# Kernel tuning notes

Measured on AMD Instinct MI355X. Metric: run time of the kernel, lower is better.

The kernel has to match this reference:

```python
import jax, jax.numpy as jnp
import numpy as np

B, D = 1024, 512


def setup_inputs() -> dict:
    key = jax.random.key(0)
    k_a, k_b, k_w, k_bias = jax.random.split(key, 4)
    a = jax.random.normal(k_a, (B, D), dtype=jnp.float32)
    b = jax.random.normal(k_b, (B, D), dtype=jnp.float32)
    # nn.Linear(input_dim, output_dim): weight [out, in], bias [out]
    bound = 1.0 / np.sqrt(D)
    W = jax.random.uniform(k_w, (D, D), dtype=jnp.float32, minval=-bound, maxval=bound)
    bias = jax.random.uniform(k_bias, (D,), dtype=jnp.float32, minval=-bound, maxval=bound)
    return {"a": a, "b": b, "W": W, "bias": bias}


def reference(a, b, W, bias):
    # attention(): weights[bt,i,j] = b[bt,i] * a[bt,j]  (rank-1 outer product, [B,D,D])
    logits = b[:, :, None] * a[:, None, :]           # [B, D, D]
    sm = jax.nn.softmax(logits, axis=1)              # softmax over dim=1 (the i axis)
    # bmm(a[B,1,D], weights^T) -> out[bt,j] = sum_k a[bt,k] * sm[bt,j,k]
    attn_out = jnp.einsum('bk,bjk->bj', a, sm)       # [B, D]
    # dropout in eval mode == identity; fc + residual
    return a + attn_out @ W.T + bias
```

## Files before the change

### kernel.cpp

```cpp
#include <hip/hip_runtime.h>

#define D 512
#define LOG2E 1.44269504088896340736f

#if defined(__has_builtin)
#if __has_builtin(__builtin_amdgcn_exp2f)
#define EXP2(x) __builtin_amdgcn_exp2f(x)
#else
#define EXP2(x) exp2f(x)
#endif
#else
#define EXP2(x) exp2f(x)
#endif

__global__ __launch_bounds__(256) void attn_kernel(
    const float* __restrict__ a, const float* __restrict__ b,
    float* __restrict__ attn) {
  __shared__ float c_s[D];
  const int bt = blockIdx.x;
  const int tid = threadIdx.x;
  const float* __restrict__ ap = a + (size_t)bt * D;
  const float* __restrict__ bp = b + (size_t)bt * D;

#pragma unroll
  for (int kk = 0; kk < 2; ++kk) {
    const int k = tid + kk * 256;
    const float ak_raw = ap[k];
    const float ak = ak_raw * LOG2E;
    float z0 = 0.f, z1 = 0.f, z2 = 0.f, z3 = 0.f;
#pragma unroll 4
    for (int i = 0; i < D; i += 4) {
      z0 += EXP2(bp[i + 0] * ak);
      z1 += EXP2(bp[i + 1] * ak);
      z2 += EXP2(bp[i + 2] * ak);
      z3 += EXP2(bp[i + 3] * ak);
    }
    c_s[k] = ak_raw / ((z0 + z1) + (z2 + z3));
  }
  __syncthreads();

#pragma unroll
  for (int jj = 0; jj < 2; ++jj) {
    const int j = tid + jj * 256;
    const float bj = bp[j] * LOG2E;
    float s0 = 0.f, s1 = 0.f, s2 = 0.f, s3 = 0.f;
#pragma unroll 4
    for (int k = 0; k < D; k += 4) {
      const float4 c4 = *(const float4*)&c_s[k];
      s0 = fmaf(c4.x, EXP2(ap[k + 0] * bj), s0);
      s1 = fmaf(c4.y, EXP2(ap[k + 1] * bj), s1);
      s2 = fmaf(c4.z, EXP2(ap[k + 2] * bj), s2);
      s3 = fmaf(c4.w, EXP2(ap[k + 3] * bj), s3);
    }
    attn[(size_t)bt * D + j] = (s0 + s1) + (s2 + s3);
  }
}

__global__ __launch_bounds__(256) void out_kernel(
    const float* __restrict__ attn, const float* __restrict__ W,
    const float* __restrict__ a, const float* __restrict__ bias,
    float* __restrict__ out) {
  __shared__ float As[32][68];
  __shared__ float Bs[32][68];
  const int tid = threadIdx.x;
  const int bx = blockIdx.x;
  const int by = blockIdx.y;
  const int tx = tid & 15;
  const int ty = tid >> 4;
  float acc[4][4] = {};

  for (int k0 = 0; k0 < D; k0 += 32) {
#pragma unroll
    for (int xx = 0; xx < 2; ++xx) {
      const int x = tid + xx * 256;
      const int r = x >> 3;
      const int c4 = x & 7;
      const float4 va =
          *(const float4*)(attn + (size_t)(by * 64 + r) * D + k0 + c4 * 4);
      const float4 vw =
          *(const float4*)(W + (size_t)(bx * 64 + r) * D + k0 + c4 * 4);
      As[c4 * 4 + 0][r] = va.x;
      As[c4 * 4 + 1][r] = va.y;
      As[c4 * 4 + 2][r] = va.z;
      As[c4 * 4 + 3][r] = va.w;
      Bs[c4 * 4 + 0][r] = vw.x;
      Bs[c4 * 4 + 1][r] = vw.y;
      Bs[c4 * 4 + 2][r] = vw.z;
      Bs[c4 * 4 + 3][r] = vw.w;
    }
    __syncthreads();
#pragma unroll
    for (int kk = 0; kk < 32; ++kk) {
      const float4 af = *(const float4*)&As[kk][ty * 4];
      const float4 bf = *(const float4*)&Bs[kk][tx * 4];
      const float afv[4] = {af.x, af.y, af.z, af.w};
      const float bfv[4] = {bf.x, bf.y, bf.z, bf.w};
#pragma unroll
      for (int i = 0; i < 4; ++i)
#pragma unroll
        for (int j = 0; j < 4; ++j) acc[i][j] = fmaf(afv[i], bfv[j], acc[i][j]);
    }
    __syncthreads();
  }

  const int n = bx * 64 + tx * 4;
  const float4 bv = *(const float4*)(bias + n);
#pragma unroll
  for (int i = 0; i < 4; ++i) {
    const int m = by * 64 + ty * 4 + i;
    const float4 av = *(const float4*)(a + (size_t)m * D + n);
    float4 o;
    o.x = av.x + acc[i][0] + bv.x;
    o.y = av.y + acc[i][1] + bv.y;
    o.z = av.z + acc[i][2] + bv.z;
    o.w = av.w + acc[i][3] + bv.w;
    *(float4*)(out + (size_t)m * D + n) = o;
  }
}

extern "C" void kernel_launch(void* const* d_in, const int* in_sizes, int n_in,
                              void* d_out, int out_size, void* d_ws,
                              size_t ws_size, hipStream_t stream) {
  const float* a = (const float*)d_in[0];
  const float* b = (const float*)d_in[1];
  const float* W = (const float*)d_in[2];
  const float* bias = (const float*)d_in[3];
  float* out = (float*)d_out;
  float* attn = (float*)d_ws;

  attn_kernel<<<1024, 256, 0, stream>>>(a, b, attn);
  out_kernel<<<dim3(8, 16), 256, 0, stream>>>(attn, W, a, bias, out);
}
```

Before: 150.6 us.

## Compute softmax exponentials once per tile in fp16 LDS; split-K GEMM with atomics

The attention kernel used to evaluate each exponential twice, once for the column sums and once for the weighted output. It now computes each exp once per 64-column tile, shifted by a bound from the max/min of b, and stores the values as half2 in swizzled shared memory. The column sums and the weighted sum then reuse those stored values, which roughly halves the transcendental work. The output GEMM is split along K into 4 slices that accumulate with atomicAdd into an output pre-filled with a+bias by a new init kernel, to raise the block count. The trade-offs are fp16 rounding of the exponentials, nondeterministic float atomics and an extra kernel launch.

```diff
diff --git a/kernel.cpp b/kernel.cpp
--- a/kernel.cpp
+++ b/kernel.cpp
@@ -1,6 +1,9 @@
 #include <hip/hip_runtime.h>
+#include <hip/hip_fp16.h>
 
 #define D 512
+#define KT 64
+#define NT 8
 #define LOG2E 1.44269504088896340736f
 
 #if defined(__has_builtin)
@@ -13,63 +16,168 @@
 #define EXP2(x) exp2f(x)
 #endif
 
-__global__ __launch_bounds__(256) void attn_kernel(
+union H2U { __half2 h; unsigned int u; };
+
+__device__ __forceinline__ unsigned int pkh(float lo, float hi) {
+  H2U p; p.h = __float22half2_rn(make_float2(lo, hi));
+  return p.u;
+}
+__device__ __forceinline__ float2 uph(unsigned int u) {
+  H2U p; p.u = u;
+  return __half22float2(p.h);
+}
+
+__global__ __launch_bounds__(256, 2) void attn_kernel(
     const float* __restrict__ a, const float* __restrict__ b,
     float* __restrict__ attn) {
-  __shared__ float c_s[D];
+  __shared__ unsigned int E[D * KT / 2];
+  __shared__ float a_s[D];
+  __shared__ float zred[32 * 68];
+  __shared__ float c_s[KT];
+  __shared__ float red[8];
+
   const int bt = blockIdx.x;
   const int tid = threadIdx.x;
   const float* __restrict__ ap = a + (size_t)bt * D;
   const float* __restrict__ bp = b + (size_t)bt * D;
 
-#pragma unroll
-  for (int kk = 0; kk < 2; ++kk) {
-    const int k = tid + kk * 256;
-    const float ak_raw = ap[k];
-    const float ak = ak_raw * LOG2E;
+  {
+    float2 va = *(const float2*)(ap + tid * 2);
+    a_s[tid * 2] = va.x;
+    a_s[tid * 2 + 1] = va.y;
+  }
+
+  const int k8 = tid & 7;
+  const int jp = tid >> 3;
+
+  float breg[16];
+#pragma unroll
+  for (int jj = 0; jj < 16; ++jj) breg[jj] = bp[jj * 32 + jp];
+
+  float bmax = breg[0], bmin = breg[0];
+#pragma unroll
+  for (int jj = 1; jj < 16; ++jj) {
+    bmax = fmaxf(bmax, breg[jj]);
+    bmin = fminf(bmin, breg[jj]);
+  }
+#pragma unroll
+  for (int off = 32; off; off >>= 1) {
+    bmax = fmaxf(bmax, __shfl_xor(bmax, off));
+    bmin = fminf(bmin, __shfl_xor(bmin, off));
+  }
+  if ((tid & 63) == 0) {
+    red[tid >> 6] = bmax;
+    red[4 + (tid >> 6)] = bmin;
+  }
+  __syncthreads();
+  bmax = fmaxf(fmaxf(red[0], red[1]), fmaxf(red[2], red[3]));
+  bmin = fminf(fminf(red[4], red[5]), fminf(red[6], red[7]));
+
+  float at0a = 0.f, at0b = 0.f, at1a = 0.f, at1b = 0.f;
+  const int jr0 = tid;
+  const int jr1 = tid + 256;
+  const int sw = jr0 & 7;
+
+  for (int t = 0; t < NT; ++t) {
+    const int k0 = t * KT;
+    float alk[8], m2[8];
+#pragma unroll
+    for (int c = 0; c < 8; ++c) {
+      const float ar = a_s[k0 + k8 * 8 + c];
+      const float al = ar * LOG2E;
+      alk[c] = al;
+      m2[c] = -al * (ar > 0.f ? bmax : bmin);
+    }
     float z0 = 0.f, z1 = 0.f, z2 = 0.f, z3 = 0.f;
-#pragma unroll 4
-    for (int i = 0; i < D; i += 4) {
-      z0 += EXP2(bp[i + 0] * ak);
-      z1 += EXP2(bp[i + 1] * ak);
-      z2 += EXP2(bp[i + 2] * ak);
-      z3 += EXP2(bp[i + 3] * ak);
-    }
-    c_s[k] = ak_raw / ((z0 + z1) + (z2 + z3));
-  }
-  __syncthreads();
-
-#pragma unroll
-  for (int jj = 0; jj < 2; ++jj) {
-    const int j = tid + jj * 256;
-    const float bj = bp[j] * LOG2E;
-    float s0 = 0.f, s1 = 0.f, s2 = 0.f, s3 = 0.f;
-#pragma unroll 4
-    for (int k = 0; k < D; k += 4) {
-      const float4 c4 = *(const float4*)&c_s[k];
-      s0 = fmaf(c4.x, EXP2(ap[k + 0] * bj), s0);
-      s1 = fmaf(c4.y, EXP2(ap[k + 1] * bj), s1);
-      s2 = fmaf(c4.z, EXP2(ap[k + 2] * bj), s2);
-      s3 = fmaf(c4.w, EXP2(ap[k + 3] * bj), s3);
-    }
-    attn[(size_t)bt * D + j] = (s0 + s1) + (s2 + s3);
-  }
-}
-
-__global__ __launch_bounds__(256) void out_kernel(
+    float z4 = 0.f, z5 = 0.f, z6 = 0.f, z7 = 0.f;
+
+#pragma unroll
+    for (int jj = 0; jj < 16; ++jj) {
+      const int j = jj * 32 + jp;
+      const float bj = breg[jj];
+      const float e0 = EXP2(fmaf(alk[0], bj, m2[0]));
+      const float e1 = EXP2(fmaf(alk[1], bj, m2[1]));
+      const float e2 = EXP2(fmaf(alk[2], bj, m2[2]));
+      const float e3 = EXP2(fmaf(alk[3], bj, m2[3]));
+      const float e4 = EXP2(fmaf(alk[4], bj, m2[4]));
+      const float e5 = EXP2(fmaf(alk[5], bj, m2[5]));
+      const float e6 = EXP2(fmaf(alk[6], bj, m2[6]));
+      const float e7 = EXP2(fmaf(alk[7], bj, m2[7]));
+      z0 += e0; z1 += e1; z2 += e2; z3 += e3;
+      z4 += e4; z5 += e5; z6 += e6; z7 += e7;
+      uint4 u;
+      u.x = pkh(e0, e1);
+      u.y = pkh(e2, e3);
+      u.z = pkh(e4, e5);
+      u.w = pkh(e6, e7);
+      *((uint4*)((char*)E + j * 128 + ((k8 ^ (j & 7)) * 16))) = u;
+    }
+    {
+      float* zp = &zred[jp * 68 + k8 * 8];
+      *(float4*)zp = make_float4(z0, z1, z2, z3);
+      *(float4*)(zp + 4) = make_float4(z4, z5, z6, z7);
+    }
+    __syncthreads();
+    if (tid < KT) {
+      float Z = 0.f;
+#pragma unroll
+      for (int p = 0; p < 32; ++p) Z += zred[p * 68 + tid];
+      c_s[tid] = a_s[k0 + tid] / Z;
+    }
+    __syncthreads();
+
+#pragma unroll
+    for (int g = 0; g < 8; ++g) {
+      const float4 c0 = *(const float4*)&c_s[g * 8];
+      const float4 c1 = *(const float4*)&c_s[g * 8 + 4];
+      const int pg = (g ^ sw) * 16;
+      const uint4 u0 = *(const uint4*)((const char*)E + jr0 * 128 + pg);
+      const uint4 u1 = *(const uint4*)((const char*)E + jr1 * 128 + pg);
+      float2 f;
+      f = uph(u0.x); at0a = fmaf(f.x, c0.x, at0a); at0b = fmaf(f.y, c0.y, at0b);
+      f = uph(u0.y); at0a = fmaf(f.x, c0.z, at0a); at0b = fmaf(f.y, c0.w, at0b);
+      f = uph(u0.z); at0a = fmaf(f.x, c1.x, at0a); at0b = fmaf(f.y, c1.y, at0b);
+      f = uph(u0.w); at0a = fmaf(f.x, c1.z, at0a); at0b = fmaf(f.y, c1.w, at0b);
+      f = uph(u1.x); at1a = fmaf(f.x, c0.x, at1a); at1b = fmaf(f.y, c0.y, at1b);
+      f = uph(u1.y); at1a = fmaf(f.x, c0.z, at1a); at1b = fmaf(f.y, c0.w, at1b);
+      f = uph(u1.z); at1a = fmaf(f.x, c1.x, at1a); at1b = fmaf(f.y, c1.y, at1b);
+      f = uph(u1.w); at1a = fmaf(f.x, c1.z, at1a); at1b = fmaf(f.y, c1.w, at1b);
+    }
+    __syncthreads();
+  }
+  attn[(size_t)bt * D + jr0] = at0a + at0b;
+  attn[(size_t)bt * D + jr1] = at1a + at1b;
+}
+
+__global__ __launch_bounds__(256) void init_out(const float* __restrict__ a,
+                                                const float* __restrict__ bias,
+                                                float* __restrict__ out) {
+  const int g = blockIdx.x * 256 + threadIdx.x;
+  const float4 av = ((const float4*)a)[g];
+  const float4 bv = ((const float4*)bias)[g & 127];
+  float4 o;
+  o.x = av.x + bv.x;
+  o.y = av.y + bv.y;
+  o.z = av.z + bv.z;
+  o.w = av.w + bv.w;
+  ((float4*)out)[g] = o;
+}
+
+__global__ __launch_bounds__(256) void gemm_kernel(
     const float* __restrict__ attn, const float* __restrict__ W,
-    const float* __restrict__ a, const float* __restrict__ bias,
     float* __restrict__ out) {
   __shared__ float As[32][68];
   __shared__ float Bs[32][68];
   const int tid = threadIdx.x;
   const int bx = blockIdx.x;
   const int by = blockIdx.y;
+  const int bz = blockIdx.z;
   const int tx = tid & 15;
   const int ty = tid >> 4;
   float acc[4][4] = {};
 
-  for (int k0 = 0; k0 < D; k0 += 32) {
+  const int kbeg = bz * 128;
+  for (int k0 = kbeg; k0 < kbeg + 128; k0 += 32) {
 #pragma unroll
     for (int xx = 0; xx < 2; ++xx) {
       const int x = tid + xx * 256;
@@ -104,17 +212,13 @@
   }
 
   const int n = bx * 64 + tx * 4;
-  const float4 bv = *(const float4*)(bias + n);
 #pragma unroll
   for (int i = 0; i < 4; ++i) {
-    const int m = by * 64 + ty * 4 + i;
-    const float4 av = *(const float4*)(a + (size_t)m * D + n);
-    float4 o;
-    o.x = av.x + acc[i][0] + bv.x;
-    o.y = av.y + acc[i][1] + bv.y;
-    o.z = av.z + acc[i][2] + bv.z;
-    o.w = av.w + acc[i][3] + bv.w;
-    *(float4*)(out + (size_t)m * D + n) = o;
+    float* op = out + (size_t)(by * 64 + ty * 4 + i) * D + n;
+    atomicAdd(op + 0, acc[i][0]);
+    atomicAdd(op + 1, acc[i][1]);
+    atomicAdd(op + 2, acc[i][2]);
+    atomicAdd(op + 3, acc[i][3]);
   }
 }
 
@@ -128,6 +232,7 @@
   float* out = (float*)d_out;
   float* attn = (float*)d_ws;
 
+  init_out<<<512, 256, 0, stream>>>(a, bias, out);
   attn_kernel<<<1024, 256, 0, stream>>>(a, b, attn);
-  out_kernel<<<dim3(8, 16), 256, 0, stream>>>(attn, W, a, bias, out);
-}
+  gemm_kernel<<<dim3(8, 16, 4), 256, 0, stream>>>(attn, W, out);
+}
```

After: 151.0 us. Within noise of the previous version (+0.2%).

## Compute each softmax exponential once and reuse for normaliser and weighted sum

Applied to the files above, without the earlier changes.

Restructures the attention kernel so each thread computes exp2 values for a 64-wide k tile, keeping them in registers. The same values feed both the column normaliser, reduced across threads through shared memory, and the weighted accumulation into output rows. This removes the second full pass of exponentials. The fc GEMM is retiled to 32x32 output tiles with 64-deep k steps, launching more blocks. In exchange there is high register pressure from the cached exponentials and extra barriers per tile.

```diff
diff --git a/kernel.cpp b/kernel.cpp
--- a/kernel.cpp
+++ b/kernel.cpp
@@ -1,6 +1,8 @@
 #include <hip/hip_runtime.h>
 
 #define D 512
+#define KT 64
+#define NT 8
 #define LOG2E 1.44269504088896340736f
 
 #if defined(__has_builtin)
@@ -13,108 +15,153 @@
 #define EXP2(x) exp2f(x)
 #endif
 
-__global__ __launch_bounds__(256) void attn_kernel(
+__global__ __launch_bounds__(256, 2) void attn_kernel(
     const float* __restrict__ a, const float* __restrict__ b,
     float* __restrict__ attn) {
-  __shared__ float c_s[D];
+  __shared__ float a_s[D];
+  __shared__ float zred[32 * 68];
+  __shared__ float c_s[KT];
+  __shared__ float attn_s[D];
+
   const int bt = blockIdx.x;
   const int tid = threadIdx.x;
   const float* __restrict__ ap = a + (size_t)bt * D;
   const float* __restrict__ bp = b + (size_t)bt * D;
 
+  {
+    float2 va = *(const float2*)(ap + tid * 2);
+    a_s[tid * 2] = va.x;
+    a_s[tid * 2 + 1] = va.y;
+  }
+
+  const int k8 = tid & 7;
+  const int jp = tid >> 3;
+
+  float breg[16];
 #pragma unroll
-  for (int kk = 0; kk < 2; ++kk) {
-    const int k = tid + kk * 256;
-    const float ak_raw = ap[k];
-    const float ak = ak_raw * LOG2E;
-    float z0 = 0.f, z1 = 0.f, z2 = 0.f, z3 = 0.f;
-#pragma unroll 4
-    for (int i = 0; i < D; i += 4) {
-      z0 += EXP2(bp[i + 0] * ak);
-      z1 += EXP2(bp[i + 1] * ak);
-      z2 += EXP2(bp[i + 2] * ak);
-      z3 += EXP2(bp[i + 3] * ak);
+  for (int jj = 0; jj < 16; ++jj) breg[jj] = bp[jj * 32 + jp];
+
+  float part[16];
+#pragma unroll
+  for (int jj = 0; jj < 16; ++jj) part[jj] = 0.f;
+
+  __syncthreads();
+
+  for (int t = 0; t < NT; ++t) {
+    const int k0 = t * KT;
+    float alk[8];
+#pragma unroll
+    for (int c = 0; c < 8; ++c) alk[c] = a_s[k0 + k8 * 8 + c] * LOG2E;
+
+    float e[16][8];
+    float z[8];
+#pragma unroll
+    for (int c = 0; c < 8; ++c) z[c] = 0.f;
+
+#pragma unroll
+    for (int jj = 0; jj < 16; ++jj) {
+      const float bj = breg[jj];
+#pragma unroll
+      for (int c = 0; c < 8; ++c) {
+        const float ev = EXP2(alk[c] * bj);
+        e[jj][c] = ev;
+        z[c] += ev;
+      }
     }
-    c_s[k] = ak_raw / ((z0 + z1) + (z2 + z3));
+    {
+      float* zp = &zred[jp * 68 + k8 * 8];
+      *(float4*)zp = make_float4(z[0], z[1], z[2], z[3]);
+      *(float4*)(zp + 4) = make_float4(z[4], z[5], z[6], z[7]);
+    }
+    __syncthreads();
+    if (tid < KT) {
+      float Z = 0.f;
+#pragma unroll
+      for (int p = 0; p < 32; ++p) Z += zred[p * 68 + tid];
+      c_s[tid] = a_s[k0 + tid] / Z;
+    }
+    __syncthreads();
+
+    float cs[8];
+    *(float4*)&cs[0] = *(const float4*)&c_s[k8 * 8];
+    *(float4*)&cs[4] = *(const float4*)&c_s[k8 * 8 + 4];
+#pragma unroll
+    for (int jj = 0; jj < 16; ++jj) {
+#pragma unroll
+      for (int c = 0; c < 8; ++c) part[jj] = fmaf(cs[c], e[jj][c], part[jj]);
+    }
+  }
+
+#pragma unroll
+  for (int jj = 0; jj < 16; ++jj) {
+    float v = part[jj];
+    v += __shfl_xor(v, 1);
+    v += __shfl_xor(v, 2);
+    v += __shfl_xor(v, 4);
+    part[jj] = v;
+  }
+  if (k8 == 0) {
+#pragma unroll
+    for (int jj = 0; jj < 16; ++jj) attn_s[jj * 32 + jp] = part[jj];
   }
   __syncthreads();
-
-#pragma unroll
-  for (int jj = 0; jj < 2; ++jj) {
-    const int j = tid + jj * 256;
-    const float bj = bp[j] * LOG2E;
-    float s0 = 0.f, s1 = 0.f, s2 = 0.f, s3 = 0.f;
-#pragma unroll 4
-    for (int k = 0; k < D; k += 4) {
-      const float4 c4 = *(const float4*)&c_s[k];
-      s0 = fmaf(c4.x, EXP2(ap[k + 0] * bj), s0);
-      s1 = fmaf(c4.y, EXP2(ap[k + 1] * bj), s1);
-      s2 = fmaf(c4.z, EXP2(ap[k + 2] * bj), s2);
-      s3 = fmaf(c4.w, EXP2(ap[k + 3] * bj), s3);
-    }
-    attn[(size_t)bt * D + j] = (s0 + s1) + (s2 + s3);
+  {
+    float2 v = *(const float2*)&attn_s[tid * 2];
+    *(float2*)(attn + (size_t)bt * D + tid * 2) = v;
   }
 }
 
-__global__ __launch_bounds__(256) void out_kernel(
+__global__ __launch_bounds__(256) void gemm_kernel(
     const float* __restrict__ attn, const float* __restrict__ W,
     const float* __restrict__ a, const float* __restrict__ bias,
     float* __restrict__ out) {
-  __shared__ float As[32][68];
-  __shared__ float Bs[32][68];
+  __shared__ float As[64][36];
+  __shared__ float Bs[64][36];
   const int tid = threadIdx.x;
   const int bx = blockIdx.x;
   const int by = blockIdx.y;
   const int tx = tid & 15;
   const int ty = tid >> 4;
-  float acc[4][4] = {};
+  const int r = tid >> 3;
+  const int c0 = (tid & 7) * 8;
+  float acc[2][2] = {};
 
-  for (int k0 = 0; k0 < D; k0 += 32) {
-#pragma unroll
-    for (int xx = 0; xx < 2; ++xx) {
-      const int x = tid + xx * 256;
-      const int r = x >> 3;
-      const int c4 = x & 7;
-      const float4 va =
-          *(const float4*)(attn + (size_t)(by * 64 + r) * D + k0 + c4 * 4);
-      const float4 vw =
-          *(const float4*)(W + (size_t)(bx * 64 + r) * D + k0 + c4 * 4);
-      As[c4 * 4 + 0][r] = va.x;
-      As[c4 * 4 + 1][r] = va.y;
-      As[c4 * 4 + 2][r] = va.z;
-      As[c4 * 4 + 3][r] = va.w;
-      Bs[c4 * 4 + 0][r] = vw.x;
-      Bs[c4 * 4 + 1][r] = vw.y;
-      Bs[c4 * 4 + 2][r] = vw.z;
-      Bs[c4 * 4 + 3][r] = vw.w;
-    }
+  for (int k0 = 0; k0 < D; k0 += 64) {
+    const float4 va0 = *(const float4*)(attn + (size_t)(by * 32 + r) * D + k0 + c0);
+    const float4 va1 = *(const float4*)(attn + (size_t)(by * 32 + r) * D + k0 + c0 + 4);
+    const float4 vw0 = *(const float4*)(W + (size_t)(bx * 32 + r) * D + k0 + c0);
+    const float4 vw1 = *(const float4*)(W + (size_t)(bx * 32 + r) * D + k0 + c0 + 4);
+    As[c0 + 0][r] = va0.x; As[c0 + 1][r] = va0.y;
+    As[c0 + 2][r] = va0.z; As[c0 + 3][r] = va0.w;
+    As[c0 + 4][r] = va1.x; As[c0 + 5][r] = va1.y;
+    As[c0 + 6][r] = va1.z; As[c0 + 7][r] = va1.w;
+    Bs[c0 + 0][r] = vw0.x; Bs[c0 + 1][r] = vw0.y;
+    Bs[c0 + 2][r] = vw0.z; Bs[c0 + 3][r] = vw0.w;
+    Bs[c0 + 4][r] = vw1.x; Bs[c0 + 5][r] = vw1.y;
+    Bs[c0 + 6][r] = vw1.z; Bs[c0 + 7][r] = vw1.w;
     __syncthreads();
-#pragma unroll
-    for (int kk = 0; kk < 32; ++kk) {
-      const float4 af = *(const float4*)&As[kk][ty * 4];
-      const float4 bf = *(const float4*)&Bs[kk][tx * 4];
-      const float afv[4] = {af.x, af.y, af.z, af.w};
-      const float bfv[4] = {bf.x, bf.y, bf.z, bf.w};
-#pragma unroll
-      for (int i = 0; i < 4; ++i)
-#pragma unroll
-        for (int j = 0; j < 4; ++j) acc[i][j] = fmaf(afv[i], bfv[j], acc[i][j]);
+#pragma unroll 16
+    for (int kk = 0; kk < 64; ++kk) {
+      const float2 af = *(const float2*)&As[kk][ty * 2];
+      const float2 bf = *(const float2*)&Bs[kk][tx * 2];
+      acc[0][0] = fmaf(af.x, bf.x, acc[0][0]);
+      acc[0][1] = fmaf(af.x, bf.y, acc[0][1]);
+      acc[1][0] = fmaf(af.y, bf.x, acc[1][0]);
+      acc[1][1] = fmaf(af.y, bf.y, acc[1][1]);
     }
     __syncthreads();
   }
 
-  const int n = bx * 64 + tx * 4;
-  const float4 bv = *(const float4*)(bias + n);
+  const int m0 = by * 32 + ty * 2;
+  const int n0 = bx * 32 + tx * 2;
+  const float2 bv = *(const float2*)&bias[n0];
 #pragma unroll
-  for (int i = 0; i < 4; ++i) {
-    const int m = by * 64 + ty * 4 + i;
-    const float4 av = *(const float4*)(a + (size_t)m * D + n);
-    float4 o;
+  for (int i = 0; i < 2; ++i) {
+    const float2 av = *(const float2*)&a[(size_t)(m0 + i) * D + n0];
+    float2 o;
     o.x = av.x + acc[i][0] + bv.x;
     o.y = av.y + acc[i][1] + bv.y;
-    o.z = av.z + acc[i][2] + bv.z;
-    o.w = av.w + acc[i][3] + bv.w;
-    *(float4*)(out + (size_t)m * D + n) = o;
+    *(float2*)(out + (size_t)(m0 + i) * D + n0) = o;
   }
 }
 
@@ -129,5 +176,5 @@
   float* attn = (float*)d_ws;
 
   attn_kernel<<<1024, 256, 0, stream>>>(a, b, attn);
-  out_kernel<<<dim3(8, 16), 256, 0, stream>>>(attn, W, a, bias, out);
+  gemm_kernel<<<dim3(16, 32), 256, 0, stream>>>(attn, W, a, bias, out);
 }
```

After: 128.7 us. 14.5% less time.
